# Performance work log

Hardware: AMD Instinct MI355X
Metric: run time of the kernel (lower is better)

The kernel has to match this reference:

```python
import jax, jax.numpy as jnp
import numpy as np


def log_g(x):
    # log(relu(x) + 0.5) for x >= 0, else -softplus(-x)
    pos = jnp.log(jnp.maximum(x, 0.0) + 0.5)
    neg = -jax.nn.softplus(-x)
    return jnp.where(x >= 0, pos, neg)


def parallel_scan_log(log_coeffs, log_values):
    # h_t = a_t * h_{t-1} + b_t, computed stably in log space
    a_star = jnp.cumsum(log_coeffs, axis=1)
    log_h0_plus_b_star = jax.lax.cumlogsumexp(log_values - a_star, axis=1)
    log_h = a_star + log_h0_plus_b_star
    return jnp.exp(log_h)


def setup_inputs() -> dict:
    key = jax.random.key(0)
    k1, k2 = jax.random.split(key)
    B, S, D = 8, 4096, 1024
    x = jax.random.normal(k1, (B, S, D), dtype=jnp.float32)
    # torch nn.Linear(dim, 2*inner_dim, bias=False): weight [2*inner_dim, dim]
    W_hg = jax.random.normal(k2, (2 * D, D), dtype=jnp.float32) * (1.0 / np.sqrt(D))
    return {"x": x, "W_hg": W_hg}


def reference(x, W_hg):
    # hidden_gate projection: [B,S,D] @ [D, 2*inner] -> [B,S,2*inner]
    hg = jnp.einsum("bsd,ed->bse", x, W_hg)
    hidden, gate = jnp.split(hg, 2, axis=-1)
    log_coeffs = -jax.nn.softplus(gate)       # log(1 - z)
    log_z = -jax.nn.softplus(-gate)           # log(z)
    log_tilde_h = log_g(hidden)
    log_values = log_z + log_tilde_h
    out = parallel_scan_log(log_coeffs, log_values)
    # expansion_factor == 1.0 -> self.out is Identity; dropout_prob == 0 -> Identity
    return out
```

## Files before the change

### kernel.cpp

```cpp
#include <hip/hip_runtime.h>

#define B_   8
#define S_   4096
#define D_   1024
#define M_   (B_ * S_)
#define N_   (2 * D_)
#define K_   D_
#define CCH  128
#define LCH  32

#define BK   32
#define NT   (K_ / BK)

typedef __attribute__((ext_vector_type(8))) short bf16x8;
typedef __attribute__((ext_vector_type(4))) float f32x4;

__device__ __forceinline__ unsigned short f2bf(float f) {
  union { float f; unsigned u; } v; v.f = f;
  unsigned u = v.u;
  u = u + 0x7fffu + ((u >> 16) & 1u);
  return (unsigned short)(u >> 16);
}
__device__ __forceinline__ float bf2f(unsigned short h) {
  union { unsigned u; float f; } v; v.u = ((unsigned)h) << 16;
  return v.f;
}
__device__ __forceinline__ float sigmoidf_(float x) {
  return 1.0f / (1.0f + __expf(-x));
}

#define GLL(src, dst) __builtin_amdgcn_global_load_lds(                     \
      (const __attribute__((address_space(1))) void*)(src),                 \
      (__attribute__((address_space(3))) void*)(dst), 16, 0, 0)

__global__ __launch_bounds__(256) void k_cvt(const float* __restrict__ in,
                                             unsigned short* __restrict__ out,
                                             int n4) {
  int i = blockIdx.x * 256 + threadIdx.x;
  const int stride = gridDim.x * 256;
  for (; i < n4; i += stride) {
    float4 v = reinterpret_cast<const float4*>(in)[i];
    ushort4 o;
    o.x = f2bf(v.x); o.y = f2bf(v.y); o.z = f2bf(v.z); o.w = f2bf(v.w);
    reinterpret_cast<ushort4*>(out)[i] = o;
  }
}

__global__ __launch_bounds__(512, 2) void k_gemm(const unsigned short* __restrict__ xb,
                                                 const unsigned short* __restrict__ wb,
                                                 unsigned short* __restrict__ Gp,
                                                 unsigned short* __restrict__ Zp) {
  __shared__ unsigned short lds[3 * 16384];
  const int tid = threadIdx.x;
  int wg = blockIdx.x;
  wg = (wg & 7) * 128 + (wg >> 3);
  const int bm = wg >> 3;
  const int bn = wg & 7;
  const int lane = tid & 63;
  const int wid = tid >> 6;
  const int wr = wid >> 2;
  const int wc = wid & 3;

  const int srow = tid >> 2;
  const int scol = (tid & 3) * 16;
  const char* agB = (const char*)xb + (size_t)(bm * 256 + srow) * 2048 + scol;
  const char* bgB = (const char*)wb + (size_t)(bn * 256 + srow) * 2048 + scol;
  unsigned short* const dst0 = &lds[srow * 32 + (tid & 3) * 8];

  f32x4 acc[8][4] = {};

  {
    const char* pa = agB;  const char* pb = bgB;
    GLL(pa, dst0);                 GLL(pa + 128 * 2048, dst0 + 4096);
    GLL(pb, dst0 + 8192);          GLL(pb + 128 * 2048, dst0 + 12288);
    pa += 64; pb += 64;
    GLL(pa, dst0 + 16384);         GLL(pa + 128 * 2048, dst0 + 20480);
    GLL(pb, dst0 + 24576);         GLL(pb + 128 * 2048, dst0 + 28672);
  }
  const char* aNext = agB + 2 * 64;
  const char* bNext = bgB + 2 * 64;

  const int fr = lane & 15;
  const int fq = (lane >> 4) * 8;
  int sl = 0;
  int sn = 2;

  for (int t = 0; t < NT - 1; ++t) {
    asm volatile("s_waitcnt vmcnt(4)\n\ts_barrier" ::: "memory");
    if (t < NT - 2) {
      unsigned short* d = dst0 + sn * 16384;
      GLL(aNext, d);                 GLL(aNext + 128 * 2048, d + 4096);
      GLL(bNext, d + 8192);          GLL(bNext + 128 * 2048, d + 12288);
      aNext += 64; bNext += 64;
    }
    const unsigned short* As = &lds[sl * 16384];
    const unsigned short* Bs = As + 8192;
    bf16x8 av[8], bv[4];
#pragma unroll
    for (int m = 0; m < 8; ++m)
      av[m] = *(const bf16x8*)&As[(wr * 128 + m * 16 + fr) * 32 + fq];
#pragma unroll
    for (int n = 0; n < 4; ++n)
      bv[n] = *(const bf16x8*)&Bs[(wc * 64 + n * 16 + fr) * 32 + fq];
    __builtin_amdgcn_s_setprio(1);
#pragma unroll
    for (int m = 0; m < 8; ++m)
#pragma unroll
      for (int n = 0; n < 4; ++n)
        acc[m][n] = __builtin_amdgcn_mfma_f32_16x16x32_bf16(av[m], bv[n], acc[m][n], 0, 0, 0);
    __builtin_amdgcn_s_setprio(0);
    sl = (sl == 2) ? 0 : sl + 1;
    sn = (sn == 2) ? 0 : sn + 1;
  }
  {
    asm volatile("s_waitcnt vmcnt(0)\n\ts_barrier" ::: "memory");
    const unsigned short* As = &lds[sl * 16384];
    const unsigned short* Bs = As + 8192;
    bf16x8 av[8], bv[4];
#pragma unroll
    for (int m = 0; m < 8; ++m)
      av[m] = *(const bf16x8*)&As[(wr * 128 + m * 16 + fr) * 32 + fq];
#pragma unroll
    for (int n = 0; n < 4; ++n)
      bv[n] = *(const bf16x8*)&Bs[(wc * 64 + n * 16 + fr) * 32 + fq];
    __builtin_amdgcn_s_setprio(1);
#pragma unroll
    for (int m = 0; m < 8; ++m)
#pragma unroll
      for (int n = 0; n < 4; ++n)
        acc[m][n] = __builtin_amdgcn_mfma_f32_16x16x32_bf16(av[m], bv[n], acc[m][n], 0, 0, 0);
    __builtin_amdgcn_s_setprio(0);
  }

  const int row0 = bm * 256 + wr * 128 + ((lane >> 4) << 2);
  const int col0 = bn * 256 + wc * 64 + fr;
  if (bn < 4) {
#pragma unroll
    for (int m = 0; m < 8; ++m)
#pragma unroll
      for (int n = 0; n < 4; ++n)
#pragma unroll
        for (int i = 0; i < 4; ++i) {
          float v = acc[m][n][i];
          float g = (v >= 0.0f) ? (v + 0.5f) : sigmoidf_(v);
          Gp[(size_t)(row0 + m * 16 + i) * 1024 + (col0 + n * 16)] = f2bf(g);
        }
  } else {
#pragma unroll
    for (int m = 0; m < 8; ++m)
#pragma unroll
      for (int n = 0; n < 4; ++n)
#pragma unroll
        for (int i = 0; i < 4; ++i) {
          float v = acc[m][n][i];
          Zp[(size_t)(row0 + m * 16 + i) * 1024 + (col0 + n * 16 - 1024)] = f2bf(sigmoidf_(v));
        }
  }
}

__global__ __launch_bounds__(256) void k_scan1(const unsigned short* __restrict__ Gp,
                                               const unsigned short* __restrict__ Zp,
                                               float* __restrict__ Ap,
                                               float* __restrict__ Hp) {
  const int gid = blockIdx.x * 256 + threadIdx.x;
  const int c = blockIdx.y;
  const int b = gid >> 8;
  const int d0 = (gid & 255) << 2;
  size_t base = ((size_t)b * S_ + (size_t)c * LCH) * 1024 + d0;
  float4 aP = {1.f, 1.f, 1.f, 1.f};
  float4 h  = {0.f, 0.f, 0.f, 0.f};
#pragma unroll 8
  for (int s = 0; s < LCH; ++s) {
    ushort4 zu = *reinterpret_cast<const ushort4*>(Zp + base);
    ushort4 gu = *reinterpret_cast<const ushort4*>(Gp + base);
    float z0 = bf2f(zu.x), z1 = bf2f(zu.y), z2 = bf2f(zu.z), z3 = bf2f(zu.w);
    float a0 = 1.f - z0,   a1 = 1.f - z1,   a2 = 1.f - z2,   a3 = 1.f - z3;
    h.x = fmaf(a0, h.x, z0 * bf2f(gu.x));
    h.y = fmaf(a1, h.y, z1 * bf2f(gu.y));
    h.z = fmaf(a2, h.z, z2 * bf2f(gu.z));
    h.w = fmaf(a3, h.w, z3 * bf2f(gu.w));
    aP.x *= a0; aP.y *= a1; aP.z *= a2; aP.w *= a3;
    base += 1024;
  }
  reinterpret_cast<float4*>(Ap)[(size_t)c * 2048 + gid] = aP;
  reinterpret_cast<float4*>(Hp)[(size_t)c * 2048 + gid] = h;
}

__global__ __launch_bounds__(256) void k_scan2(const float* __restrict__ Ap,
                                               const float* __restrict__ Hp,
                                               float* __restrict__ Cin) {
  const int gid = blockIdx.x * 256 + threadIdx.x;
  float4 carry = {0.f, 0.f, 0.f, 0.f};
  for (int c = 0; c < CCH; ++c) {
    reinterpret_cast<float4*>(Cin)[(size_t)c * 2048 + gid] = carry;
    float4 a = reinterpret_cast<const float4*>(Ap)[(size_t)c * 2048 + gid];
    float4 hh = reinterpret_cast<const float4*>(Hp)[(size_t)c * 2048 + gid];
    carry.x = fmaf(a.x, carry.x, hh.x);
    carry.y = fmaf(a.y, carry.y, hh.y);
    carry.z = fmaf(a.z, carry.z, hh.z);
    carry.w = fmaf(a.w, carry.w, hh.w);
  }
}

__global__ __launch_bounds__(256) void k_scan3(const unsigned short* __restrict__ Gp,
                                               const unsigned short* __restrict__ Zp,
                                               const float* __restrict__ Cin,
                                               float* __restrict__ out) {
  const int gid = blockIdx.x * 256 + threadIdx.x;
  const int c = blockIdx.y;
  const int b = gid >> 8;
  const int d0 = (gid & 255) << 2;
  size_t base = ((size_t)b * S_ + (size_t)c * LCH) * 1024 + d0;
  float4 h = reinterpret_cast<const float4*>(Cin)[(size_t)c * 2048 + gid];
#pragma unroll 8
  for (int s = 0; s < LCH; ++s) {
    ushort4 zu = *reinterpret_cast<const ushort4*>(Zp + base);
    ushort4 gu = *reinterpret_cast<const ushort4*>(Gp + base);
    float z0 = bf2f(zu.x), z1 = bf2f(zu.y), z2 = bf2f(zu.z), z3 = bf2f(zu.w);
    h.x = fmaf(1.f - z0, h.x, z0 * bf2f(gu.x));
    h.y = fmaf(1.f - z1, h.y, z1 * bf2f(gu.y));
    h.z = fmaf(1.f - z2, h.z, z2 * bf2f(gu.z));
    h.w = fmaf(1.f - z3, h.w, z3 * bf2f(gu.w));
    *reinterpret_cast<float4*>(out + base) = h;
    base += 1024;
  }
}

extern "C" void kernel_launch(void* const* d_in, const int* in_sizes, int n_in,
                              void* d_out, int out_size, void* d_ws, size_t ws_size,
                              hipStream_t stream) {
  const float* x = (const float*)d_in[0];
  const float* W = (const float*)d_in[1];
  float* out = (float*)d_out;

  unsigned char* w = (unsigned char*)d_ws;
  unsigned short* xb = (unsigned short*)(w);
  unsigned short* wb = (unsigned short*)(w + 67108864);
  unsigned short* Gp = (unsigned short*)(w + 67108864 + 4194304);
  unsigned short* Zp = (unsigned short*)(w + 67108864 + 4194304 + 67108864);
  float* Ap  = (float*)(w);
  float* Hp  = (float*)(w + 4194304);
  float* Cin = (float*)(w + 8388608);

  k_cvt<<<4096, 256, 0, stream>>>(x, xb, (M_ * K_) / 4);
  k_cvt<<<2048, 256, 0, stream>>>(W, wb, (N_ * K_) / 4);
  k_gemm<<<(M_ / 256) * (N_ / 256), 512, 0, stream>>>(xb, wb, Gp, Zp);
  k_scan1<<<dim3(8, CCH), 256, 0, stream>>>(Gp, Zp, Ap, Hp);
  k_scan2<<<8, 256, 0, stream>>>(Ap, Hp, Cin);
  k_scan3<<<dim3(8, CCH), 256, 0, stream>>>(Gp, Zp, Cin, out);
}
```

Baseline: 277.0 us.

## Double K tile to 64 with XOR-swizzled LDS and interleaved prefetch

The GEMM main loop moves from a triple-buffered BK=32 pipeline to a double-buffered BK=64 pipeline. The LDS layout now uses an XOR swizzle on 16-byte blocks to avoid bank conflicts, and the global-to-LDS loads for the next tile are issued in pieces between MFMA phases. This halves the number of barriers per K and hides load issue behind compute. The cost is 128KB of LDS per block, which may limit occupancy to one block per CU despite launch_bounds(512,2), plus an extra barrier in each iteration.

```diff
diff --git a/kernel.cpp b/kernel.cpp
--- a/kernel.cpp
+++ b/kernel.cpp
@@ -9,7 +9,7 @@
 #define CCH  128
 #define LCH  32
 
-#define BK   32
+#define BK   64
 #define NT   (K_ / BK)
 
 typedef __attribute__((ext_vector_type(8))) short bf16x8;
@@ -50,7 +50,7 @@
                                                  const unsigned short* __restrict__ wb,
                                                  unsigned short* __restrict__ Gp,
                                                  unsigned short* __restrict__ Zp) {
-  __shared__ unsigned short lds[3 * 16384];
+  __shared__ unsigned short lds[65536];
   const int tid = threadIdx.x;
   int wg = blockIdx.x;
   wg = (wg & 7) * 128 + (wg >> 3);
@@ -60,79 +60,82 @@
   const int wid = tid >> 6;
   const int wr = wid >> 2;
   const int wc = wid & 3;
-
-  const int srow = tid >> 2;
-  const int scol = (tid & 3) * 16;
-  const char* agB = (const char*)xb + (size_t)(bm * 256 + srow) * 2048 + scol;
-  const char* bgB = (const char*)wb + (size_t)(bn * 256 + srow) * 2048 + scol;
-  unsigned short* const dst0 = &lds[srow * 32 + (tid & 3) * 8];
+  const int fr = lane & 15;
+  const int hi = lane >> 4;
+  const int f7 = fr & 7;
+
+  const int srow = tid >> 3;
+  const int sblk = tid & 7;
+  const int scol = ((sblk ^ (srow & 7)) * 16);
+  const char* aS = (const char*)xb + (size_t)(bm * 256 + srow) * 2048 + scol;
+  const char* bS = (const char*)wb + (size_t)(bn * 256 + srow) * 2048 + scol;
+  char* const ldsc = (char*)lds + (size_t)tid * 16;
+
+#define STAGE_PAIR(srcbase, kbyte, bufbyte, region, C0)                      \
+  GLL((srcbase) + (size_t)(C0) * 131072 + (kbyte),                           \
+      ldsc + (bufbyte) + (region) + (C0) * 8192);                            \
+  GLL((srcbase) + (size_t)((C0) + 1) * 131072 + (kbyte),                     \
+      ldsc + (bufbyte) + (region) + ((C0) + 1) * 8192)
 
   f32x4 acc[8][4] = {};
-
-  {
-    const char* pa = agB;  const char* pb = bgB;
-    GLL(pa, dst0);                 GLL(pa + 128 * 2048, dst0 + 4096);
-    GLL(pb, dst0 + 8192);          GLL(pb + 128 * 2048, dst0 + 12288);
-    pa += 64; pb += 64;
-    GLL(pa, dst0 + 16384);         GLL(pa + 128 * 2048, dst0 + 20480);
-    GLL(pb, dst0 + 24576);         GLL(pb + 128 * 2048, dst0 + 28672);
-  }
-  const char* aNext = agB + 2 * 64;
-  const char* bNext = bgB + 2 * 64;
-
-  const int fr = lane & 15;
-  const int fq = (lane >> 4) * 8;
-  int sl = 0;
-  int sn = 2;
-
-  for (int t = 0; t < NT - 1; ++t) {
-    asm volatile("s_waitcnt vmcnt(4)\n\ts_barrier" ::: "memory");
-    if (t < NT - 2) {
-      unsigned short* d = dst0 + sn * 16384;
-      GLL(aNext, d);                 GLL(aNext + 128 * 2048, d + 4096);
-      GLL(bNext, d + 8192);          GLL(bNext + 128 * 2048, d + 12288);
-      aNext += 64; bNext += 64;
-    }
-    const unsigned short* As = &lds[sl * 16384];
-    const unsigned short* Bs = As + 8192;
-    bf16x8 av[8], bv[4];
-#pragma unroll
-    for (int m = 0; m < 8; ++m)
-      av[m] = *(const bf16x8*)&As[(wr * 128 + m * 16 + fr) * 32 + fq];
-#pragma unroll
-    for (int n = 0; n < 4; ++n)
-      bv[n] = *(const bf16x8*)&Bs[(wc * 64 + n * 16 + fr) * 32 + fq];
-    __builtin_amdgcn_s_setprio(1);
-#pragma unroll
-    for (int m = 0; m < 8; ++m)
-#pragma unroll
-      for (int n = 0; n < 4; ++n)
-        acc[m][n] = __builtin_amdgcn_mfma_f32_16x16x32_bf16(av[m], bv[n], acc[m][n], 0, 0, 0);
-    __builtin_amdgcn_s_setprio(0);
-    sl = (sl == 2) ? 0 : sl + 1;
-    sn = (sn == 2) ? 0 : sn + 1;
-  }
-  {
-    asm volatile("s_waitcnt vmcnt(0)\n\ts_barrier" ::: "memory");
-    const unsigned short* As = &lds[sl * 16384];
-    const unsigned short* Bs = As + 8192;
-    bf16x8 av[8], bv[4];
-#pragma unroll
-    for (int m = 0; m < 8; ++m)
-      av[m] = *(const bf16x8*)&As[(wr * 128 + m * 16 + fr) * 32 + fq];
-#pragma unroll
-    for (int n = 0; n < 4; ++n)
-      bv[n] = *(const bf16x8*)&Bs[(wc * 64 + n * 16 + fr) * 32 + fq];
-    __builtin_amdgcn_s_setprio(1);
-#pragma unroll
-    for (int m = 0; m < 8; ++m)
-#pragma unroll
-      for (int n = 0; n < 4; ++n)
-        acc[m][n] = __builtin_amdgcn_mfma_f32_16x16x32_bf16(av[m], bv[n], acc[m][n], 0, 0, 0);
-    __builtin_amdgcn_s_setprio(0);
-  }
-
-  const int row0 = bm * 256 + wr * 128 + ((lane >> 4) << 2);
+  bf16x8 av[8], bv[4];
+
+  STAGE_PAIR(aS, 0, 0, 0, 0);       STAGE_PAIR(aS, 0, 0, 0, 2);
+  STAGE_PAIR(bS, 0, 0, 32768, 0);   STAGE_PAIR(bS, 0, 0, 32768, 2);
+  STAGE_PAIR(aS, 128, 65536, 0, 0);     STAGE_PAIR(aS, 128, 65536, 0, 2);
+  STAGE_PAIR(bS, 128, 65536, 32768, 0); STAGE_PAIR(bS, 128, 65536, 32768, 2);
+
+  const int swz0 = (hi ^ f7) * 8;
+  const int swz1 = ((4 + hi) ^ f7) * 8;
+
+#define LOAD_FRAGS(Ab, Bb, SWZ)                                              \
+  _Pragma("unroll") for (int m = 0; m < 8; ++m)                              \
+    av[m] = *(const bf16x8*)&(Ab)[(wr * 128 + m * 16 + fr) * 64 + (SWZ)];    \
+  _Pragma("unroll") for (int n = 0; n < 4; ++n)                              \
+    bv[n] = *(const bf16x8*)&(Bb)[(wc * 64 + n * 16 + fr) * 64 + (SWZ)];
+
+#define PHASE(M0)                                                            \
+  __builtin_amdgcn_s_setprio(1);                                             \
+  _Pragma("unroll") for (int m = (M0); m < (M0) + 2; ++m)                    \
+    _Pragma("unroll") for (int n = 0; n < 4; ++n)                            \
+      acc[m][n] = __builtin_amdgcn_mfma_f32_16x16x32_bf16(av[m], bv[n],      \
+                                                          acc[m][n], 0, 0, 0); \
+  __builtin_amdgcn_s_setprio(0);
+
+#define PHASE4(M0)                                                           \
+  __builtin_amdgcn_s_setprio(1);                                             \
+  _Pragma("unroll") for (int m = (M0); m < (M0) + 4; ++m)                    \
+    _Pragma("unroll") for (int n = 0; n < 4; ++n)                            \
+      acc[m][n] = __builtin_amdgcn_mfma_f32_16x16x32_bf16(av[m], bv[n],      \
+                                                          acc[m][n], 0, 0, 0); \
+  __builtin_amdgcn_s_setprio(0);
+
+  for (int t = 0; t < NT; ++t) {
+    if (t < NT - 1) asm volatile("s_waitcnt vmcnt(8)\n\ts_barrier" ::: "memory");
+    else            asm volatile("s_waitcnt vmcnt(0)\n\ts_barrier" ::: "memory");
+
+    const unsigned short* Ab = &lds[(t & 1) << 15];
+    const unsigned short* Bb = Ab + 16384;
+    const int bufbyte = (t & 1) * 65536;
+    const size_t kbyte = (size_t)(t + 2) * 128;
+
+    LOAD_FRAGS(Ab, Bb, swz0);
+    PHASE4(0);
+    PHASE4(4);
+    LOAD_FRAGS(Ab, Bb, swz1);
+    asm volatile("s_waitcnt lgkmcnt(0)\n\ts_barrier" ::: "memory");
+
+    if (t < NT - 2) { STAGE_PAIR(aS, kbyte, bufbyte, 0, 0); }
+    PHASE(0);
+    if (t < NT - 2) { STAGE_PAIR(aS, kbyte, bufbyte, 0, 2); }
+    PHASE(2);
+    if (t < NT - 2) { STAGE_PAIR(bS, kbyte, bufbyte, 32768, 0); }
+    PHASE(4);
+    if (t < NT - 2) { STAGE_PAIR(bS, kbyte, bufbyte, 32768, 2); }
+    PHASE(6);
+  }
+
+  const int row0 = bm * 256 + wr * 128 + (hi << 2);
   const int col0 = bn * 256 + wc * 64 + fr;
   if (bn < 4) {
 #pragma unroll
```

Result: faster. 265.2 us (-4.2%).
